# Optimization experiments

Measured on AMD Instinct MI355X. Metric: run time of the kernel, lower is better.

## Reference

```python
import jax, jax.numpy as jnp
import numpy as np

B, N = 32, 512
N_DIM, N_P, N_K = 128, 3, 2
F0_DIM = N_DIM * N_P            # 384
CAT_DIM = N_DIM * (N_K + 1) * N_P  # 1152


def setup_inputs() -> dict:
    key = jax.random.key(0)
    ks = jax.random.split(key, 12)
    s = 0.05
    return {
        "loc": jax.random.uniform(ks[0], (B, N, 2), dtype=jnp.float32),
        "deadline": jax.random.uniform(ks[1], (B, N), dtype=jnp.float32),
        "workload": jax.random.uniform(ks[2], (B, N), dtype=jnp.float32),
        "depot": jax.random.uniform(ks[3], (B, 1, 2), dtype=jnp.float32),
        "W_init": jax.random.normal(ks[4], (3, F0_DIM), dtype=jnp.float32) * s,
        "b_init": jnp.zeros((F0_DIM,), jnp.float32),
        "W_dep": jax.random.normal(ks[5], (2, N_DIM), dtype=jnp.float32) * s,
        "b_dep": jnp.zeros((N_DIM,), jnp.float32),
        "W_g1": jax.random.normal(ks[6], (CAT_DIM, N_DIM), dtype=jnp.float32) * s,
        "b_g1": jnp.zeros((N_DIM,), jnp.float32),
        "W_g2": jax.random.normal(ks[7], (CAT_DIM, N_DIM), dtype=jnp.float32) * s,
        "b_g2": jnp.zeros((N_DIM,), jnp.float32),
        "W_g3": jax.random.normal(ks[8], (CAT_DIM, N_DIM), dtype=jnp.float32) * s,
        "b_g3": jnp.zeros((N_DIM,), jnp.float32),
        "gamma": jnp.ones((F0_DIM,), jnp.float32),
        "beta": jnp.zeros((F0_DIM,), jnp.float32),
        "W_F": jax.random.normal(ks[9], (F0_DIM, N_DIM), dtype=jnp.float32) * s,
        "b_F": jnp.zeros((N_DIM,), jnp.float32),
    }


def _forward(loc, deadline, workload, depot, W_init, b_init, W_dep, b_dep,
             W_g1, b_g1, W_g2, b_g2, W_g3, b_g3, gamma, beta, W_F, b_F):
    # X = [loc, deadline/deadline.max()] -> [B,N,3] (workload is concatenated then dropped in original)
    X = jnp.concatenate([loc, (deadline / deadline.max())[..., None]], axis=-1)
    n = X.shape[1]
    # pairwise squared distances [B,N,N]
    d2 = ((X[:, :, None, :] - X[:, None, :, :]) ** 2).sum(-1)
    off = ~jnp.eye(n, dtype=bool)                      # off-diagonal mask
    d2_safe = jnp.where(off, d2, 1.0)
    A = jnp.where(off, 1.0 / jnp.sqrt(d2_safe), 0.0)   # A = 1/dist off-diag, 0 on diag
    A = jnp.where(jnp.isnan(A), 0.0, A)                # A[A!=A]=0
    A = A / A.max()                                    # global max-normalize
    deg = A.sum(-1) - 1.0                              # (A.sum(-1) - 1)
    L = jnp.eye(n, dtype=A.dtype) * deg[:, None, :] - A  # D - A (diag = deg)
    L2 = L @ L

    F0 = X @ W_init + b_init                           # [B,N,384]
    F0_sq = F0 * F0
    F0_cu = F0 * F0_sq

    def prop(F):
        return jnp.concatenate([F, L @ F, L2 @ F], axis=-1)  # [B,N,1152]

    g1 = prop(F0) @ W_g1 + b_g1
    g2 = prop(F0_sq) @ W_g2 + b_g2
    g3 = prop(F0_cu) @ W_g3 + b_g3
    F1 = jnp.concatenate([g1, g2, g3], axis=-1)        # [B,N,384]
    F1 = jax.nn.leaky_relu(F1) + F0

    # BatchNorm1d (training mode): stats over flattened (B*N) samples, biased var
    flat = F1.reshape(-1, F1.shape[-1])
    mu = flat.mean(0)
    var = ((flat - mu) ** 2).mean(0)
    F1 = (F1 - mu) / jnp.sqrt(var + 1e-5) * gamma + beta

    F_final = jax.nn.leaky_relu(F1 @ W_F + b_F)        # [B,N,128]
    dep = depot @ W_dep + b_dep                        # [B,1,128]
    h = jnp.concatenate([dep, F_final], axis=1)        # [B,N+1,128]
    return h, h.mean(axis=1)


def reference(loc, deadline, workload, depot, W_init, b_init, W_dep, b_dep,
              W_g1, b_g1, W_g2, b_g2, W_g3, b_g3, gamma, beta, W_F, b_F):
    return _forward(loc, deadline, workload, depot, W_init, b_init, W_dep, b_dep,
                    W_g1, b_g1, W_g2, b_g2, W_g3, b_g3, gamma, beta, W_F, b_F)
```

## Files before the change

kernel.cpp:

```cpp
#include <hip/hip_runtime.h>

#define LEAKY(x) ((x) > 0.0f ? (x) : 0.01f * (x))

typedef __attribute__((ext_vector_type(8))) short bf16x8;
typedef __attribute__((ext_vector_type(4))) float f32x4;
typedef __attribute__((ext_vector_type(8))) unsigned short u16x8;
typedef __attribute__((ext_vector_type(4))) unsigned short u16x4;

__device__ __forceinline__ unsigned short f2bf(float f) {
    unsigned int u = __float_as_uint(f);
    unsigned int r = (u + 0x7fffu + ((u >> 16) & 1u)) >> 16;
    return (unsigned short)r;
}
__device__ __forceinline__ float bf2f(unsigned short u) {
    return __uint_as_float(((unsigned int)u) << 16);
}

#define GLD16(gp, lp) __builtin_amdgcn_global_load_lds( \
    (__attribute__((address_space(1))) void*)(gp), \
    (__attribute__((address_space(3))) void*)(lp), 16, 0, 0)


__global__ void k_dmax(const float* __restrict__ deadline, float* __restrict__ dmax) {
    int t = threadIdx.x;
// ... 35 lines not shown
    if (threadIdx.x == 0) {
        float m = fmaxf(fmaxf(smax[0], smax[1]), fmaxf(smax[2], smax[3]));
        atomicMax((unsigned int*)(pmax64 + (blk & 63)), __float_as_uint(m));
    }
}

__global__ __launch_bounds__(256) void k_build(
    const float* __restrict__ loc, const float* __restrict__ deadline,
    const float* __restrict__ dmaxv, const float* __restrict__ rowsum,
    const float* __restrict__ pmax64,
    const float* __restrict__ Wi, const float* __restrict__ bi_,
    const float* __restrict__ Wg1, const float* __restrict__ Wg2, const float* __restrict__ Wg3,
    unsigned short* __restrict__ Lb,
    unsigned short* __restrict__ P1, unsigned short* __restrict__ P2, unsigned short* __restrict__ P3,
    unsigned short* __restrict__ WgT)
{
    __shared__ float amaxS;
    int blk = blockIdx.x;
    int t = threadIdx.x;
    if (blk < 8192) {
        if (t < 64) {
            float m = pmax64[t];
            for (int off = 32; off > 0; off >>= 1) m = fmaxf(m, __shfl_down(m, off));
            if (t == 0) amaxS = m;
        }
        __syncthreads();
        float inv = 1.0f / amaxS;
        float invd = 1.0f / (*dmaxv);
        int id = blk * 256 + t;
        size_t e = (size_t)id * 4;
        size_t bi = e >> 9;
        int b = (int)(bi >> 9);
        int i = (int)(bi & 511);
        int j0 = (int)(e & 511);
        const float* lb = loc + b * 1024;
        const float* db = deadline + b * 512;
        float xi = lb[i * 2], yi = lb[i * 2 + 1], zi = db[i] * invd;
        float4 l01 = *(const float4*)(lb + j0 * 2);
        float4 l23 = *(const float4*)(lb + j0 * 2 + 4);
        float4 dj = *(const float4*)(db + j0);
        float diag = rowsum[bi] * inv - 1.0f;
        float jx[4] = {l01.x, l01.z, l23.x, l23.z};
        float jy[4] = {l01.y, l01.w, l23.y, l23.w};
        float jz[4] = {dj.x * invd, dj.y * invd, dj.z * invd, dj.w * invd};
        u16x4 o;
#pragma unroll
        for (int j = 0; j < 4; j++) {
            float d0 = xi - jx[j], d1 = yi - jy[j], d2 = zi - jz[j];
            float dd = d0 * d0 + d1 * d1 + d2 * d2;
            float v = (i == j0 + j) ? diag : -rsqrtf(dd) * inv;
            o[j] = f2bf(v);
        }
        *(u16x4*)(Lb + e) = o;
    } else if (blk < 14336) {
        int id = (blk - 8192) * 256 + t;
        int row = id / 96, c4 = (id % 96) * 4;
        float x0 = loc[row * 2], x1 = loc[row * 2 + 1], x2 = deadline[row] / (*dmaxv);
        float4 w0 = *(const float4*)(Wi + c4);
        float4 w1 = *(const float4*)(Wi + 384 + c4);
        float4 w2 = *(const float4*)(Wi + 768 + c4);
        float4 bb = *(const float4*)(bi_ + c4);
        float f[4] = {x0 * w0.x + x1 * w1.x + x2 * w2.x + bb.x,
                      x0 * w0.y + x1 * w1.y + x2 * w2.y + bb.y,
                      x0 * w0.z + x1 * w1.z + x2 * w2.z + bb.z,
                      x0 * w0.w + x1 * w1.w + x2 * w2.w + bb.w};
        u16x4 o1, o2, o3;
#pragma unroll
        for (int j = 0; j < 4; j++) {
            o1[j] = f2bf(f[j]); o2[j] = f2bf(f[j] * f[j]); o3[j] = f2bf(f[j] * f[j] * f[j]);
        }
        size_t e = (size_t)row * 384 + c4;
        *(u16x4*)(P1 + e) = o1; *(u16x4*)(P2 + e) = o2; *(u16x4*)(P3 + e) = o3;
    } else {
        int id = (blk - 14336) * 256 + t;
        int part = id / 147456, rem = id % 147456;
        int g = rem / 384, k = rem % 384;
        int kp = g >> 7, n = g & 127;
        const float* W = (kp == 0) ? Wg1 : (kp == 1 ? Wg2 : Wg3);
        WgT[id] = f2bf(W[(part * 384 + k) * 128 + n]);
    }
}


__device__ __forceinline__ void pipe128x128(
    const unsigned short* __restrict__ A0, int As0, const unsigned short* __restrict__ B0, int Bs0, int it0,
    const unsigned short* __restrict__ A1, int As1, const unsigned short* __restrict__ B1, int Bs1, int it1,
    unsigned short* AsL, unsigned short* BsL,
    f32x4 (&acc)[4][4], int t)
{
    const int lane = t & 63, wave = t >> 6;
    const int wm = wave >> 1, wn = wave & 1;
    const int quad = lane >> 4, l16 = lane & 15;
    const int lrow = lane >> 3;
    const int lsw  = ((lane & 7) ^ lrow) * 8;
    const int total = it0 + it1;

    auto stage = [&](int buf, int s) {
        int sg = (s >= it0);
        const unsigned short* A = sg ? A1 : A0;
        const unsigned short* B = sg ? B1 : B0;
        int As = sg ? As1 : As0, Bs = sg ? Bs1 : Bs0;
        int k0 = (sg ? (s - it0) : s) * 64;
#pragma unroll
        for (int j = 0; j < 4; j++) {
            int r0 = wave * 32 + j * 8;
            GLD16(A + (size_t)(r0 + lrow) * As + k0 + lsw, AsL + buf * 8192 + r0 * 64);
            GLD16(B + (size_t)(r0 + lrow) * Bs + k0 + lsw, BsL + buf * 8192 + r0 * 64);
        }
    };

    stage(0, 0);
    if (total > 1) stage(1, 1);
    for (int s = 0; s < total; s++) {
        const int buf = s & 1;
        if (s + 1 < total) asm volatile("s_waitcnt vmcnt(8)" ::: "memory");
        else               asm volatile("s_waitcnt vmcnt(0)" ::: "memory");
        __builtin_amdgcn_s_barrier();
        __builtin_amdgcn_sched_barrier(0);
        bf16x8 af[2][4], bfr[2][4];
#pragma unroll
        for (int h = 0; h < 2; h++) {
            int phys = ((h * 4 + quad) ^ (l16 & 7)) * 8;
#pragma unroll
            for (int i = 0; i < 4; i++)
                af[h][i] = *(const bf16x8*)(AsL + buf * 8192 + (wm * 64 + i * 16 + l16) * 64 + phys);
#pragma unroll
            for (int n = 0; n < 4; n++)
                bfr[h][n] = *(const bf16x8*)(BsL + buf * 8192 + (wn * 64 + n * 16 + l16) * 64 + phys);
        }
        asm volatile("s_waitcnt lgkmcnt(0)" ::: "memory");
        __builtin_amdgcn_sched_barrier(0);
        __builtin_amdgcn_s_barrier();
        __builtin_amdgcn_sched_barrier(0);
        if (s + 2 < total) stage(buf, s + 2);
#pragma unroll
        for (int h = 0; h < 2; h++)
#pragma unroll
            for (int i = 0; i < 4; i++)
#pragma unroll
                for (int n = 0; n < 4; n++)
                    acc[i][n] = __builtin_amdgcn_mfma_f32_16x16x32_bf16(af[h][i], bfr[h][n], acc[i][n], 0, 0, 0);
    }
}

__device__ __forceinline__ void pipe64x64(
    const unsigned short* __restrict__ A0, int As0, const unsigned short* __restrict__ B0, int Bs0, int it0,
    unsigned short* AsL, unsigned short* BsL,
    f32x4 (&acc)[2][2], int t)
{
    const int lane = t & 63, wave = t >> 6;
    const int wm = wave >> 1, wn = wave & 1;
    const int quad = lane >> 4, l16 = lane & 15;
    const int lrow = lane >> 3;
    const int lsw  = ((lane & 7) ^ lrow) * 8;

    auto stage = [&](int buf, int s) {
        int k0 = s * 64;
#pragma unroll
        for (int j = 0; j < 2; j++) {
            int r0 = wave * 16 + j * 8;
            GLD16(A0 + (size_t)(r0 + lrow) * As0 + k0 + lsw, AsL + buf * 4096 + r0 * 64);
            GLD16(B0 + (size_t)(r0 + lrow) * Bs0 + k0 + lsw, BsL + buf * 4096 + r0 * 64);
        }
    };

    stage(0, 0);
    if (it0 > 1) stage(1, 1);
    for (int s = 0; s < it0; s++) {
        const int buf = s & 1;
        if (s + 1 < it0) asm volatile("s_waitcnt vmcnt(4)" ::: "memory");
        else             asm volatile("s_waitcnt vmcnt(0)" ::: "memory");
        __builtin_amdgcn_s_barrier();
        __builtin_amdgcn_sched_barrier(0);
        bf16x8 af[2][2], bfr[2][2];
#pragma unroll
        for (int h = 0; h < 2; h++) {
            int phys = ((h * 4 + quad) ^ (l16 & 7)) * 8;
#pragma unroll
            for (int i = 0; i < 2; i++)
                af[h][i] = *(const bf16x8*)(AsL + buf * 4096 + (wm * 32 + i * 16 + l16) * 64 + phys);
#pragma unroll
            for (int n = 0; n < 2; n++)
                bfr[h][n] = *(const bf16x8*)(BsL + buf * 4096 + (wn * 32 + n * 16 + l16) * 64 + phys);
        }
        asm volatile("s_waitcnt lgkmcnt(0)" ::: "memory");
        __builtin_amdgcn_sched_barrier(0);
        __builtin_amdgcn_s_barrier();
        __builtin_amdgcn_sched_barrier(0);
        if (s + 2 < it0) stage(buf, s + 2);
#pragma unroll
        for (int h = 0; h < 2; h++)
#pragma unroll
            for (int i = 0; i < 2; i++)
#pragma unroll
                for (int n = 0; n < 2; n++)
                    acc[i][n] = __builtin_amdgcn_mfma_f32_16x16x32_bf16(af[h][i], bfr[h][n], acc[i][n], 0, 0, 0);
    }
}

__global__ __launch_bounds__(256) void k_ygemmT(
    const unsigned short* __restrict__ WgT,
    const unsigned short* __restrict__ P1, const unsigned short* __restrict__ P2,
    const unsigned short* __restrict__ P3, unsigned short* __restrict__ Y2T)
{
    __shared__ unsigned short AsL[16384], BsL[16384];
    const int t = threadIdx.x;
    const int id = blockIdx.x;
    const int b = id & 31, tt = id >> 5;
    const int kp = tt >> 2, nb = tt & 3;
    const unsigned short* P = (kp == 0) ? P1 : (kp == 1 ? P2 : P3);
    f32x4 acc[4][4];
#pragma unroll
    for (int i = 0; i < 4; i++)
#pragma unroll
        for (int n = 0; n < 4; n++) acc[i][n] = (f32x4){0.f, 0.f, 0.f, 0.f};
    pipe128x128(WgT + ((size_t)2 * 384 + kp * 128) * 384, 384,
                P + ((size_t)b * 512 + nb * 128) * 384, 384, 6,
                nullptr, 0, nullptr, 0, 0, AsL, BsL, acc, t);

    const int wave = t >> 6, lane = t & 63;
    const int wm = wave >> 1, wn = wave & 1;
    const int quad = lane >> 4, l16 = lane & 15;
#pragma unroll
    for (int i = 0; i < 4; i++)
#pragma unroll
        for (int n = 0; n < 4; n++) {
            int g = kp * 128 + wm * 64 + i * 16 + quad * 4;
            int node = nb * 128 + wn * 64 + n * 16 + l16;
#pragma unroll
            for (int r = 0; r < 4; r++)
                Y2T[((size_t)b * 384 + g + r) * 512 + node] = f2bf(acc[i][n][r]);
        }
}

__global__ __launch_bounds__(256) void k_lg1T(
    const unsigned short* __restrict__ Lb, const unsigned short* __restrict__ Y2T,
    const unsigned short* __restrict__ WgT,
    const unsigned short* __restrict__ P1, const unsigned short* __restrict__ P2,
    const unsigned short* __restrict__ P3, unsigned short* __restrict__ ZT)
{
    __shared__ unsigned short AsL[16384], BsL[16384];
    const int t = threadIdx.x;
    const int id = blockIdx.x;
    const int b = id & 31, tt = id >> 5;
    const int kp = tt >> 2, nb = tt & 3;
    const unsigned short* P = (kp == 0) ? P1 : (kp == 1 ? P2 : P3);
    f32x4 acc[4][4];
#pragma unroll
    for (int i = 0; i < 4; i++)
#pragma unroll
        for (int n = 0; n < 4; n++) acc[i][n] = (f32x4){0.f, 0.f, 0.f, 0.f};
    pipe128x128(Y2T + (size_t)b * 196608 + (size_t)kp * 128 * 512, 512,
                Lb + (size_t)b * 262144 + (size_t)nb * 128 * 512, 512, 8,
                WgT + ((size_t)1 * 384 + kp * 128) * 384, 384,
                P + ((size_t)b * 512 + nb * 128) * 384, 384, 6, AsL, BsL, acc, t);

    const int wave = t >> 6, lane = t & 63;
    const int wm = wave >> 1, wn = wave & 1;
    const int quad = lane >> 4, l16 = lane & 15;
#pragma unroll
    for (int i = 0; i < 4; i++)
#pragma unroll
        for (int n = 0; n < 4; n++) {
            int g = kp * 128 + wm * 64 + i * 16 + quad * 4;
            int node = nb * 128 + wn * 64 + n * 16 + l16;
#pragma unroll
            for (int r = 0; r < 4; r++)
                ZT[((size_t)b * 384 + g + r) * 512 + node] = f2bf(acc[i][n][r]);
        }
}

__global__ __launch_bounds__(256) void k_lg2(
    const unsigned short* __restrict__ Lb, const unsigned short* __restrict__ ZT,
    const unsigned short* __restrict__ WgT,
    const unsigned short* __restrict__ P1, const unsigned short* __restrict__ P2,
    const unsigned short* __restrict__ P3,
    const float* __restrict__ bg1, const float* __restrict__ bg2, const float* __restrict__ bg3,
    unsigned short* __restrict__ F1b, float* __restrict__ bn1, float* __restrict__ bn2)
{
    __shared__ unsigned short AsL[16384], BsL[16384];
    __shared__ float bnS[128], bnQ[128];
    const int t = threadIdx.x;
    const int id = blockIdx.x;
    const int b = id & 31, tt = id >> 5;
    const int mb = tt & 3, gt = tt >> 2;
    if (t < 128) { bnS[t] = 0.f; bnQ[t] = 0.f; }
    const unsigned short* P = (gt == 0) ? P1 : (gt == 1 ? P2 : P3);
    f32x4 acc[4][4];
#pragma unroll
    for (int i = 0; i < 4; i++)
#pragma unroll
        for (int n = 0; n < 4; n++) acc[i][n] = (f32x4){0.f, 0.f, 0.f, 0.f};
    pipe128x128(Lb + (size_t)b * 262144 + (size_t)mb * 128 * 512, 512,
                ZT + (size_t)b * 196608 + (size_t)gt * 128 * 512, 512, 8,
                P + ((size_t)b * 512 + mb * 128) * 384, 384,
                WgT + (size_t)(gt * 128) * 384, 384, 6,
                AsL, BsL, acc, t);

    const int wave = t >> 6, lane = t & 63;
    const int wm = wave >> 1, wn = wave & 1;
    const int quad = lane >> 4, l16 = lane & 15;
    const float* bg = (gt == 0) ? bg1 : (gt == 1 ? bg2 : bg3);
    float ls1[4], ls2[4];
#pragma unroll
    for (int n = 0; n < 4; n++) { ls1[n] = 0.f; ls2[n] = 0.f; }
#pragma unroll
    for (int i = 0; i < 4; i++) {
        int rowl = mb * 128 + wm * 64 + i * 16 + quad * 4;
        size_t rowg = (size_t)b * 512 + rowl;
#pragma unroll
        for (int n = 0; n < 4; n++) {
            int nloc = wn * 64 + n * 16 + l16;
            int g = gt * 128 + nloc;
            float bias = bg[nloc];
#pragma unroll
            for (int r = 0; r < 4; r++) {
                size_t idx = (rowg + r) * 384 + g;
                float c = acc[i][n][r] + bias;
                float v = LEAKY(c) + bf2f(P1[idx]);
                F1b[idx] = f2bf(v);
                ls1[n] += v; ls2[n] += v * v;
            }
        }
    }
#pragma unroll
    for (int n = 0; n < 4; n++) {
        int nloc = wn * 64 + n * 16 + l16;
        atomicAdd(&bnS[nloc], ls1[n]);
        atomicAdd(&bnQ[nloc], ls2[n]);
    }
    __syncthreads();
    if (t < 128) {
        atomicAdd(&bn1[gt * 128 + t], bnS[t]);
        atomicAdd(&bn2[gt * 128 + t], bnQ[t]);
    }
}

__global__ __launch_bounds__(256) void k_bnfold(
    const float* __restrict__ bn1, const float* __restrict__ bn2,
    const float* __restrict__ gamma, const float* __restrict__ beta,
    const float* __restrict__ WF, const float* __restrict__ bF,
    unsigned short* __restrict__ WFsT, float* __restrict__ beffv)
{
    int blk = blockIdx.x;
    if (blk < 192) {
        int id = blk * 256 + threadIdx.x;
        int n = id / 384, k = id % 384;
        float mu = bn1[k] * (1.f / 16384.f);
        float var = bn2[k] * (1.f / 16384.f) - mu * mu;
        float sc = gamma[k] / sqrtf(var + 1e-5f);
        WFsT[id] = f2bf(WF[k * 128 + n] * sc);
    } else {
        __shared__ float ttL[384];
        int c = threadIdx.x;
        for (int k = c; k < 384; k += 256) {
            float mu = bn1[k] * (1.f / 16384.f);
            float var = bn2[k] * (1.f / 16384.f) - mu * mu;
            float sc = gamma[k] / sqrtf(var + 1e-5f);
            ttL[k] = beta[k] - mu * sc;
        }
        __syncthreads();
        if (c < 128) {
            float a = bF[c];
            for (int k = 0; k < 384; k++) a += ttL[k] * WF[k * 128 + c];
            beffv[c] = a;
        }
    }
}

__global__ __launch_bounds__(256) void k_fgemm(
    const unsigned short* __restrict__ F1b, const unsigned short* __restrict__ WFsT,
    const float* __restrict__ beffv, float* __restrict__ out, float* __restrict__ msum)
{
    __shared__ unsigned short AsL[8192], BsL[8192];
    __shared__ float msS[64];
    const int t = threadIdx.x;
    const int id = blockIdx.x;
    const int b = id & 31, tt = id >> 5;
    const int seg = tt >> 1, nt = tt & 1;
    if (t < 64) msS[t] = 0.f;
    f32x4 acc[2][2];
#pragma unroll
    for (int i = 0; i < 2; i++)
#pragma unroll
        for (int n = 0; n < 2; n++) acc[i][n] = (f32x4){0.f, 0.f, 0.f, 0.f};
    pipe64x64(F1b + ((size_t)b * 512 + seg * 64) * 384, 384,
              WFsT + (size_t)nt * 64 * 384, 384, 6, AsL, BsL, acc, t);

    const int wave = t >> 6, lane = t & 63;
    const int wm = wave >> 1, wn = wave & 1;
    const int quad = lane >> 4, l16 = lane & 15;
    float ls[2];
#pragma unroll
    for (int n = 0; n < 2; n++) ls[n] = 0.f;
#pragma unroll
    for (int i = 0; i < 2; i++) {
        int nd = seg * 64 + wm * 32 + i * 16 + quad * 4;
#pragma unroll
        for (int n = 0; n < 2; n++) {
            int col = nt * 64 + wn * 32 + n * 16 + l16;
            float bb = beffv[col];
#pragma unroll
            for (int r = 0; r < 4; r++) {
                float x = acc[i][n][r] + bb;
                float v = LEAKY(x);
                out[(size_t)b * 65664 + (size_t)(nd + r + 1) * 128 + col] = v;
                ls[n] += v;
            }
        }
    }
#pragma unroll
    for (int n = 0; n < 2; n++) atomicAdd(&msS[wn * 32 + n * 16 + l16], ls[n]);
    __syncthreads();
    if (t < 64) atomicAdd(&msum[b * 128 + nt * 64 + t], msS[t]);
}

__global__ void k_meandep(const float* __restrict__ depot, const float* __restrict__ Wd,
                          const float* __restrict__ bd, const float* __restrict__ msum,
                          float* __restrict__ out) {
    int id = blockIdx.x * 256 + threadIdx.x;
    int b = id >> 7, o = id & 127;
    float dep = depot[b * 2] * Wd[o] + depot[b * 2 + 1] * Wd[128 + o] + bd[o];
    out[(size_t)b * 65664 + o] = dep;
    out[2101248 + id] = (msum[id] + dep) * (1.0f / 513.0f);
}


extern "C" void kernel_launch(void* const* d_in, const int* in_sizes, int n_in,
                              void* d_out, int out_size, void* d_ws, size_t ws_size,
                              hipStream_t stream) {
    const float* loc      = (const float*)d_in[0];
    const float* deadline = (const float*)d_in[1];
    const float* depot    = (const float*)d_in[3];
    const float* W_init   = (const float*)d_in[4];
    const float* b_init   = (const float*)d_in[5];
    const float* W_dep    = (const float*)d_in[6];
    const float* b_dep    = (const float*)d_in[7];
    const float* W_g1     = (const float*)d_in[8];
    const float* b_g1     = (const float*)d_in[9];
    const float* W_g2     = (const float*)d_in[10];
    const float* b_g2     = (const float*)d_in[11];
    const float* W_g3     = (const float*)d_in[12];
    const float* b_g3     = (const float*)d_in[13];
    const float* gamma    = (const float*)d_in[14];
    const float* beta     = (const float*)d_in[15];
    const float* W_F      = (const float*)d_in[16];
    const float* b_F      = (const float*)d_in[17];
    float* out = (float*)d_out;
    float* ws  = (float*)d_ws;

    float* dmaxv  = ws + 0;
    float* pmax64 = ws + 4;
    float* bn1    = ws + 68;
    float* bn2    = ws + 452;
    float* msum   = ws + 836;
    float* rowsum = ws + 4932;
    float* beffv  = ws + 21316;
    unsigned short* Lb   = (unsigned short*)(ws + 21448);
    unsigned short* P1   = (unsigned short*)(ws + 4215752);
    unsigned short* P2   = (unsigned short*)(ws + 7361480);
    unsigned short* P3   = (unsigned short*)(ws + 10507208);
    unsigned short* WgT  = (unsigned short*)(ws + 13652936);
    unsigned short* WFsT = (unsigned short*)(ws + 13874120);
    unsigned short* Y2T  = (unsigned short*)(ws + 13898696);
    unsigned short* ZT   = (unsigned short*)(ws + 17044424);
    unsigned short* F1b  = (unsigned short*)(ws + 20190152);

    hipMemsetAsync(ws, 0, 4932 * sizeof(float), stream);

    k_dmax<<<64, 256, 0, stream>>>(deadline, dmaxv);
    k_rowstats<<<4096, 256, 0, stream>>>(loc, deadline, dmaxv, rowsum, pmax64);
    k_build<<<16064, 256, 0, stream>>>(loc, deadline, dmaxv, rowsum, pmax64,
                                       W_init, b_init, W_g1, W_g2, W_g3,
                                       Lb, P1, P2, P3, WgT);

    k_ygemmT<<<384, 256, 0, stream>>>(WgT, P1, P2, P3, Y2T);
    k_lg1T<<<384, 256, 0, stream>>>(Lb, Y2T, WgT, P1, P2, P3, ZT);
    k_lg2<<<384, 256, 0, stream>>>(Lb, ZT, WgT, P1, P2, P3,
                                   b_g1, b_g2, b_g3, F1b, bn1, bn2);

    k_bnfold<<<193, 256, 0, stream>>>(bn1, bn2, gamma, beta, W_F, b_F, WFsT, beffv);
    k_fgemm<<<512, 256, 0, stream>>>(F1b, WFsT, beffv, out, msum);
    k_meandep<<<16, 256, 0, stream>>>(depot, W_dep, b_dep, msum, out);
}
```

Measured before the change: 222.6 us.

## Split 128x128 GEMM tiles across 8 waves with MFMA operand swap and setprio

The three graph-propagation GEMM kernels now launch 512 threads (8 waves) per 128x128 tile instead of 256. Each wave computes a 32x64 sub-tile and issues half as many global-to-LDS loads per stage, with the vmcnt waits adjusted to match. For the transposed-output kernels, the MFMA operands are swapped so each lane holds four consecutive nodes, which allows a single vectorized 4-element bf16 store in place of four strided scalar stores. s_setprio is raised around the MFMA bursts to favour the math waves over the load-issuing ones. The aim is better latency hiding with only 384 blocks on the device, at the cost of lower per-wave register reuse and more barrier participants.

```diff
diff --git a/kernel.cpp b/kernel.cpp
--- a/kernel.cpp
+++ b/kernel.cpp
@@ -141,11 +141,12 @@
 }
 
 
+template <bool SWAP>
 __device__ __forceinline__ void pipe128x128(
     const unsigned short* __restrict__ A0, int As0, const unsigned short* __restrict__ B0, int Bs0, int it0,
     const unsigned short* __restrict__ A1, int As1, const unsigned short* __restrict__ B1, int Bs1, int it1,
     unsigned short* AsL, unsigned short* BsL,
-    f32x4 (&acc)[4][4], int t)
+    f32x4 (&acc)[2][4], int t)
 {
     const int lane = t & 63, wave = t >> 6;
     const int wm = wave >> 1, wn = wave & 1;
@@ -161,8 +162,8 @@
         int As = sg ? As1 : As0, Bs = sg ? Bs1 : Bs0;
         int k0 = (sg ? (s - it0) : s) * 64;
 #pragma unroll
-        for (int j = 0; j < 4; j++) {
-            int r0 = wave * 32 + j * 8;
+        for (int j = 0; j < 2; j++) {
+            int r0 = wave * 16 + j * 8;
             GLD16(A + (size_t)(r0 + lrow) * As + k0 + lsw, AsL + buf * 8192 + r0 * 64);
             GLD16(B + (size_t)(r0 + lrow) * Bs + k0 + lsw, BsL + buf * 8192 + r0 * 64);
         }
@@ -172,17 +173,17 @@
     if (total > 1) stage(1, 1);
     for (int s = 0; s < total; s++) {
         const int buf = s & 1;
-        if (s + 1 < total) asm volatile("s_waitcnt vmcnt(8)" ::: "memory");
+        if (s + 1 < total) asm volatile("s_waitcnt vmcnt(4)" ::: "memory");
         else               asm volatile("s_waitcnt vmcnt(0)" ::: "memory");
         __builtin_amdgcn_s_barrier();
         __builtin_amdgcn_sched_barrier(0);
-        bf16x8 af[2][4], bfr[2][4];
+        bf16x8 af[2][2], bfr[2][4];
 #pragma unroll
         for (int h = 0; h < 2; h++) {
             int phys = ((h * 4 + quad) ^ (l16 & 7)) * 8;
 #pragma unroll
-            for (int i = 0; i < 4; i++)
-                af[h][i] = *(const bf16x8*)(AsL + buf * 8192 + (wm * 64 + i * 16 + l16) * 64 + phys);
+            for (int i = 0; i < 2; i++)
+                af[h][i] = *(const bf16x8*)(AsL + buf * 8192 + (wm * 32 + i * 16 + l16) * 64 + phys);
 #pragma unroll
             for (int n = 0; n < 4; n++)
                 bfr[h][n] = *(const bf16x8*)(BsL + buf * 8192 + (wn * 64 + n * 16 + l16) * 64 + phys);
@@ -192,13 +193,17 @@
         __builtin_amdgcn_s_barrier();
         __builtin_amdgcn_sched_barrier(0);
         if (s + 2 < total) stage(buf, s + 2);
+        __builtin_amdgcn_s_setprio(1);
 #pragma unroll
         for (int h = 0; h < 2; h++)
 #pragma unroll
-            for (int i = 0; i < 4; i++)
+            for (int i = 0; i < 2; i++)
 #pragma unroll
                 for (int n = 0; n < 4; n++)
-                    acc[i][n] = __builtin_amdgcn_mfma_f32_16x16x32_bf16(af[h][i], bfr[h][n], acc[i][n], 0, 0, 0);
+                    acc[i][n] = SWAP
+                        ? __builtin_amdgcn_mfma_f32_16x16x32_bf16(bfr[h][n], af[h][i], acc[i][n], 0, 0, 0)
+                        : __builtin_amdgcn_mfma_f32_16x16x32_bf16(af[h][i], bfr[h][n], acc[i][n], 0, 0, 0);
+        __builtin_amdgcn_s_setprio(0);
     }
 }
 
@@ -247,6 +252,7 @@
         __builtin_amdgcn_s_barrier();
         __builtin_amdgcn_sched_barrier(0);
         if (s + 2 < it0) stage(buf, s + 2);
+        __builtin_amdgcn_s_setprio(1);
 #pragma unroll
         for (int h = 0; h < 2; h++)
 #pragma unroll
@@ -254,10 +260,11 @@
 #pragma unroll
                 for (int n = 0; n < 2; n++)
                     acc[i][n] = __builtin_amdgcn_mfma_f32_16x16x32_bf16(af[h][i], bfr[h][n], acc[i][n], 0, 0, 0);
-    }
-}
-
-__global__ __launch_bounds__(256) void k_ygemmT(
+        __builtin_amdgcn_s_setprio(0);
+    }
+}
+
+__global__ __launch_bounds__(512, 4) void k_ygemmT(
     const unsigned short* __restrict__ WgT,
     const unsigned short* __restrict__ P1, const unsigned short* __restrict__ P2,
     const unsigned short* __restrict__ P3, unsigned short* __restrict__ Y2T)
@@ -268,31 +275,33 @@
     const int b = id & 31, tt = id >> 5;
     const int kp = tt >> 2, nb = tt & 3;
     const unsigned short* P = (kp == 0) ? P1 : (kp == 1 ? P2 : P3);
-    f32x4 acc[4][4];
-#pragma unroll
-    for (int i = 0; i < 4; i++)
+    f32x4 acc[2][4];
+#pragma unroll
+    for (int i = 0; i < 2; i++)
 #pragma unroll
         for (int n = 0; n < 4; n++) acc[i][n] = (f32x4){0.f, 0.f, 0.f, 0.f};
-    pipe128x128(WgT + ((size_t)2 * 384 + kp * 128) * 384, 384,
-                P + ((size_t)b * 512 + nb * 128) * 384, 384, 6,
-                nullptr, 0, nullptr, 0, 0, AsL, BsL, acc, t);
+    pipe128x128<true>(WgT + ((size_t)2 * 384 + kp * 128) * 384, 384,
+                      P + ((size_t)b * 512 + nb * 128) * 384, 384, 6,
+                      nullptr, 0, nullptr, 0, 0, AsL, BsL, acc, t);
 
     const int wave = t >> 6, lane = t & 63;
     const int wm = wave >> 1, wn = wave & 1;
     const int quad = lane >> 4, l16 = lane & 15;
 #pragma unroll
-    for (int i = 0; i < 4; i++)
+    for (int i = 0; i < 2; i++) {
+        int g = kp * 128 + wm * 32 + i * 16 + l16;
 #pragma unroll
         for (int n = 0; n < 4; n++) {
-            int g = kp * 128 + wm * 64 + i * 16 + quad * 4;
-            int node = nb * 128 + wn * 64 + n * 16 + l16;
-#pragma unroll
-            for (int r = 0; r < 4; r++)
-                Y2T[((size_t)b * 384 + g + r) * 512 + node] = f2bf(acc[i][n][r]);
-        }
-}
-
-__global__ __launch_bounds__(256) void k_lg1T(
+            int node = nb * 128 + wn * 64 + n * 16 + quad * 4;
+            u16x4 o;
+#pragma unroll
+            for (int r = 0; r < 4; r++) o[r] = f2bf(acc[i][n][r]);
+            *(u16x4*)(Y2T + ((size_t)b * 384 + g) * 512 + node) = o;
+        }
+    }
+}
+
+__global__ __launch_bounds__(512, 4) void k_lg1T(
     const unsigned short* __restrict__ Lb, const unsigned short* __restrict__ Y2T,
     const unsigned short* __restrict__ WgT,
     const unsigned short* __restrict__ P1, const unsigned short* __restrict__ P2,
@@ -304,32 +313,34 @@
     const int b = id & 31, tt = id >> 5;
     const int kp = tt >> 2, nb = tt & 3;
     const unsigned short* P = (kp == 0) ? P1 : (kp == 1 ? P2 : P3);
-    f32x4 acc[4][4];
-#pragma unroll
-    for (int i = 0; i < 4; i++)
+    f32x4 acc[2][4];
+#pragma unroll
+    for (int i = 0; i < 2; i++)
 #pragma unroll
         for (int n = 0; n < 4; n++) acc[i][n] = (f32x4){0.f, 0.f, 0.f, 0.f};
-    pipe128x128(Y2T + (size_t)b * 196608 + (size_t)kp * 128 * 512, 512,
-                Lb + (size_t)b * 262144 + (size_t)nb * 128 * 512, 512, 8,
-                WgT + ((size_t)1 * 384 + kp * 128) * 384, 384,
-                P + ((size_t)b * 512 + nb * 128) * 384, 384, 6, AsL, BsL, acc, t);
+    pipe128x128<true>(Y2T + (size_t)b * 196608 + (size_t)kp * 128 * 512, 512,
+                      Lb + (size_t)b * 262144 + (size_t)nb * 128 * 512, 512, 8,
+                      WgT + ((size_t)1 * 384 + kp * 128) * 384, 384,
+                      P + ((size_t)b * 512 + nb * 128) * 384, 384, 6, AsL, BsL, acc, t);
 
     const int wave = t >> 6, lane = t & 63;
     const int wm = wave >> 1, wn = wave & 1;
     const int quad = lane >> 4, l16 = lane & 15;
 #pragma unroll
-    for (int i = 0; i < 4; i++)
+    for (int i = 0; i < 2; i++) {
+        int g = kp * 128 + wm * 32 + i * 16 + l16;
 #pragma unroll
         for (int n = 0; n < 4; n++) {
-            int g = kp * 128 + wm * 64 + i * 16 + quad * 4;
-            int node = nb * 128 + wn * 64 + n * 16 + l16;
-#pragma unroll
-            for (int r = 0; r < 4; r++)
-                ZT[((size_t)b * 384 + g + r) * 512 + node] = f2bf(acc[i][n][r]);
-        }
-}
-
-__global__ __launch_bounds__(256) void k_lg2(
+            int node = nb * 128 + wn * 64 + n * 16 + quad * 4;
+            u16x4 o;
+#pragma unroll
+            for (int r = 0; r < 4; r++) o[r] = f2bf(acc[i][n][r]);
+            *(u16x4*)(ZT + ((size_t)b * 384 + g) * 512 + node) = o;
+        }
+    }
+}
+
+__global__ __launch_bounds__(512, 4) void k_lg2(
     const unsigned short* __restrict__ Lb, const unsigned short* __restrict__ ZT,
     const unsigned short* __restrict__ WgT,
     const unsigned short* __restrict__ P1, const unsigned short* __restrict__ P2,
@@ -345,16 +356,16 @@
     const int mb = tt & 3, gt = tt >> 2;
     if (t < 128) { bnS[t] = 0.f; bnQ[t] = 0.f; }
     const unsigned short* P = (gt == 0) ? P1 : (gt == 1 ? P2 : P3);
-    f32x4 acc[4][4];
-#pragma unroll
-    for (int i = 0; i < 4; i++)
+    f32x4 acc[2][4];
+#pragma unroll
+    for (int i = 0; i < 2; i++)
 #pragma unroll
         for (int n = 0; n < 4; n++) acc[i][n] = (f32x4){0.f, 0.f, 0.f, 0.f};
-    pipe128x128(Lb + (size_t)b * 262144 + (size_t)mb * 128 * 512, 512,
-                ZT + (size_t)b * 196608 + (size_t)gt * 128 * 512, 512, 8,
-                P + ((size_t)b * 512 + mb * 128) * 384, 384,
-                WgT + (size_t)(gt * 128) * 384, 384, 6,
-                AsL, BsL, acc, t);
+    pipe128x128<false>(Lb + (size_t)b * 262144 + (size_t)mb * 128 * 512, 512,
+                       ZT + (size_t)b * 196608 + (size_t)gt * 128 * 512, 512, 8,
+                       P + ((size_t)b * 512 + mb * 128) * 384, 384,
+                       WgT + (size_t)(gt * 128) * 384, 384, 6,
+                       AsL, BsL, acc, t);
 
     const int wave = t >> 6, lane = t & 63;
     const int wm = wave >> 1, wn = wave & 1;
@@ -364,8 +375,8 @@
 #pragma unroll
     for (int n = 0; n < 4; n++) { ls1[n] = 0.f; ls2[n] = 0.f; }
 #pragma unroll
-    for (int i = 0; i < 4; i++) {
-        int rowl = mb * 128 + wm * 64 + i * 16 + quad * 4;
+    for (int i = 0; i < 2; i++) {
+        int rowl = mb * 128 + wm * 32 + i * 16 + quad * 4;
         size_t rowg = (size_t)b * 512 + rowl;
 #pragma unroll
         for (int n = 0; n < 4; n++) {
@@ -533,9 +544,9 @@
                                        W_init, b_init, W_g1, W_g2, W_g3,
                                        Lb, P1, P2, P3, WgT);
 
-    k_ygemmT<<<384, 256, 0, stream>>>(WgT, P1, P2, P3, Y2T);
-    k_lg1T<<<384, 256, 0, stream>>>(Lb, Y2T, WgT, P1, P2, P3, ZT);
-    k_lg2<<<384, 256, 0, stream>>>(Lb, ZT, WgT, P1, P2, P3,
+    k_ygemmT<<<384, 512, 0, stream>>>(WgT, P1, P2, P3, Y2T);
+    k_lg1T<<<384, 512, 0, stream>>>(Lb, Y2T, WgT, P1, P2, P3, ZT);
+    k_lg2<<<384, 512, 0, stream>>>(Lb, ZT, WgT, P1, P2, P3,
                                    b_g1, b_g2, b_g3, F1b, bn1, bn2);
 
     k_bnfold<<<193, 256, 0, stream>>>(bn1, bn2, gamma, beta, W_F, b_F, WFsT, beffv);
```

Measured after the change: 230.5 us. +3.5%, slower.

## Precompute all three weight-projection products in one launch and add them in epilogues

Applied to the files above, without the earlier changes.

All three W·P projections (parts 0, 1 and 2) now come from a single wider kernel, k_wp, with 1152 blocks. The Laplacian GEMMs therefore no longer chain a second K-segment through the pipeline. They add the precomputed Y1/Y0 terms in their epilogues, and swapped MFMA operand order gives vectorized u16x4 stores. This removes the dual-segment pipeline logic and lets the weight GEMMs run with more parallelism. In exchange it adds extra global writes and reads of two bf16 intermediates (Y1T aliases F1b, Y0T is a new buffer) and an additional bf16 rounding before the sum.

```diff
diff --git a/kernel.cpp b/kernel.cpp
--- a/kernel.cpp
+++ b/kernel.cpp
@@ -141,9 +141,9 @@
 }
 
 
+template <bool SWAP>
 __device__ __forceinline__ void pipe128x128(
     const unsigned short* __restrict__ A0, int As0, const unsigned short* __restrict__ B0, int Bs0, int it0,
-    const unsigned short* __restrict__ A1, int As1, const unsigned short* __restrict__ B1, int Bs1, int it1,
     unsigned short* AsL, unsigned short* BsL,
     f32x4 (&acc)[4][4], int t)
 {
@@ -152,28 +152,23 @@
     const int quad = lane >> 4, l16 = lane & 15;
     const int lrow = lane >> 3;
     const int lsw  = ((lane & 7) ^ lrow) * 8;
-    const int total = it0 + it1;
 
     auto stage = [&](int buf, int s) {
-        int sg = (s >= it0);
-        const unsigned short* A = sg ? A1 : A0;
-        const unsigned short* B = sg ? B1 : B0;
-        int As = sg ? As1 : As0, Bs = sg ? Bs1 : Bs0;
-        int k0 = (sg ? (s - it0) : s) * 64;
+        int k0 = s * 64;
 #pragma unroll
         for (int j = 0; j < 4; j++) {
             int r0 = wave * 32 + j * 8;
-            GLD16(A + (size_t)(r0 + lrow) * As + k0 + lsw, AsL + buf * 8192 + r0 * 64);
-            GLD16(B + (size_t)(r0 + lrow) * Bs + k0 + lsw, BsL + buf * 8192 + r0 * 64);
+            GLD16(A0 + (size_t)(r0 + lrow) * As0 + k0 + lsw, AsL + buf * 8192 + r0 * 64);
+            GLD16(B0 + (size_t)(r0 + lrow) * Bs0 + k0 + lsw, BsL + buf * 8192 + r0 * 64);
         }
     };
 
     stage(0, 0);
-    if (total > 1) stage(1, 1);
-    for (int s = 0; s < total; s++) {
+    if (it0 > 1) stage(1, 1);
+    for (int s = 0; s < it0; s++) {
         const int buf = s & 1;
-        if (s + 1 < total) asm volatile("s_waitcnt vmcnt(8)" ::: "memory");
-        else               asm volatile("s_waitcnt vmcnt(0)" ::: "memory");
+        if (s + 1 < it0) asm volatile("s_waitcnt vmcnt(8)" ::: "memory");
+        else             asm volatile("s_waitcnt vmcnt(0)" ::: "memory");
         __builtin_amdgcn_s_barrier();
         __builtin_amdgcn_sched_barrier(0);
         bf16x8 af[2][4], bfr[2][4];
@@ -191,14 +186,16 @@
         __builtin_amdgcn_sched_barrier(0);
         __builtin_amdgcn_s_barrier();
         __builtin_amdgcn_sched_barrier(0);
-        if (s + 2 < total) stage(buf, s + 2);
+        if (s + 2 < it0) stage(buf, s + 2);
 #pragma unroll
         for (int h = 0; h < 2; h++)
 #pragma unroll
             for (int i = 0; i < 4; i++)
 #pragma unroll
                 for (int n = 0; n < 4; n++)
-                    acc[i][n] = __builtin_amdgcn_mfma_f32_16x16x32_bf16(af[h][i], bfr[h][n], acc[i][n], 0, 0, 0);
+                    acc[i][n] = SWAP
+                        ? __builtin_amdgcn_mfma_f32_16x16x32_bf16(bfr[h][n], af[h][i], acc[i][n], 0, 0, 0)
+                        : __builtin_amdgcn_mfma_f32_16x16x32_bf16(af[h][i], bfr[h][n], acc[i][n], 0, 0, 0);
     }
 }
 
@@ -257,83 +254,88 @@
     }
 }
 
-__global__ __launch_bounds__(256) void k_ygemmT(
+__global__ __launch_bounds__(256) void k_wp(
     const unsigned short* __restrict__ WgT,
     const unsigned short* __restrict__ P1, const unsigned short* __restrict__ P2,
-    const unsigned short* __restrict__ P3, unsigned short* __restrict__ Y2T)
+    const unsigned short* __restrict__ P3,
+    unsigned short* __restrict__ Y0T, unsigned short* __restrict__ Y1T,
+    unsigned short* __restrict__ Y2T)
+{
+    __shared__ unsigned short AsL[16384], BsL[16384];
+    const int t = threadIdx.x;
+    const int id = blockIdx.x;
+    const int b = id & 31, tt = id >> 5;
+    const int kp = tt / 12, rem = tt % 12;
+    const int part = rem >> 2, nb = rem & 3;
+    const unsigned short* P = (kp == 0) ? P1 : (kp == 1 ? P2 : P3);
+    unsigned short* Y = (part == 2) ? Y2T : (part == 1 ? Y1T : Y0T);
+    f32x4 acc[4][4];
+#pragma unroll
+    for (int i = 0; i < 4; i++)
+#pragma unroll
+        for (int n = 0; n < 4; n++) acc[i][n] = (f32x4){0.f, 0.f, 0.f, 0.f};
+    pipe128x128<true>(WgT + ((size_t)part * 384 + kp * 128) * 384, 384,
+                      P + ((size_t)b * 512 + nb * 128) * 384, 384, 6,
+                      AsL, BsL, acc, t);
+
+    const int wave = t >> 6, lane = t & 63;
+    const int wm = wave >> 1, wn = wave & 1;
+    const int quad = lane >> 4, l16 = lane & 15;
+#pragma unroll
+    for (int i = 0; i < 4; i++) {
+        int g = kp * 128 + wm * 64 + i * 16 + l16;
+#pragma unroll
+        for (int n = 0; n < 4; n++) {
+            int node = nb * 128 + wn * 64 + n * 16 + quad * 4;
+            u16x4 o;
+#pragma unroll
+            for (int r = 0; r < 4; r++) o[r] = f2bf(acc[i][n][r]);
+            *(u16x4*)(Y + ((size_t)b * 384 + g) * 512 + node) = o;
+        }
+    }
+}
+
+__global__ __launch_bounds__(256) void k_lg1T(
+    const unsigned short* __restrict__ Lb, const unsigned short* __restrict__ Y2T,
+    const unsigned short* __restrict__ Y1T, unsigned short* __restrict__ ZT)
 {
     __shared__ unsigned short AsL[16384], BsL[16384];
     const int t = threadIdx.x;
     const int id = blockIdx.x;
     const int b = id & 31, tt = id >> 5;
     const int kp = tt >> 2, nb = tt & 3;
-    const unsigned short* P = (kp == 0) ? P1 : (kp == 1 ? P2 : P3);
     f32x4 acc[4][4];
 #pragma unroll
     for (int i = 0; i < 4; i++)
 #pragma unroll
         for (int n = 0; n < 4; n++) acc[i][n] = (f32x4){0.f, 0.f, 0.f, 0.f};
-    pipe128x128(WgT + ((size_t)2 * 384 + kp * 128) * 384, 384,
-                P + ((size_t)b * 512 + nb * 128) * 384, 384, 6,
-                nullptr, 0, nullptr, 0, 0, AsL, BsL, acc, t);
+    pipe128x128<true>(Y2T + (size_t)b * 196608 + (size_t)kp * 128 * 512, 512,
+                      Lb + (size_t)b * 262144 + (size_t)nb * 128 * 512, 512, 8,
+                      AsL, BsL, acc, t);
 
     const int wave = t >> 6, lane = t & 63;
     const int wm = wave >> 1, wn = wave & 1;
     const int quad = lane >> 4, l16 = lane & 15;
 #pragma unroll
-    for (int i = 0; i < 4; i++)
+    for (int i = 0; i < 4; i++) {
+        int g = kp * 128 + wm * 64 + i * 16 + l16;
 #pragma unroll
         for (int n = 0; n < 4; n++) {
-            int g = kp * 128 + wm * 64 + i * 16 + quad * 4;
-            int node = nb * 128 + wn * 64 + n * 16 + l16;
-#pragma unroll
-            for (int r = 0; r < 4; r++)
-                Y2T[((size_t)b * 384 + g + r) * 512 + node] = f2bf(acc[i][n][r]);
-        }
-}
-
-__global__ __launch_bounds__(256) void k_lg1T(
-    const unsigned short* __restrict__ Lb, const unsigned short* __restrict__ Y2T,
-    const unsigned short* __restrict__ WgT,
-    const unsigned short* __restrict__ P1, const unsigned short* __restrict__ P2,
-    const unsigned short* __restrict__ P3, unsigned short* __restrict__ ZT)
-{
-    __shared__ unsigned short AsL[16384], BsL[16384];
-    const int t = threadIdx.x;
-    const int id = blockIdx.x;
-    const int b = id & 31, tt = id >> 5;
-    const int kp = tt >> 2, nb = tt & 3;
-    const unsigned short* P = (kp == 0) ? P1 : (kp == 1 ? P2 : P3);
-    f32x4 acc[4][4];
-#pragma unroll
-    for (int i = 0; i < 4; i++)
-#pragma unroll
-        for (int n = 0; n < 4; n++) acc[i][n] = (f32x4){0.f, 0.f, 0.f, 0.f};
-    pipe128x128(Y2T + (size_t)b * 196608 + (size_t)kp * 128 * 512, 512,
-                Lb + (size_t)b * 262144 + (size_t)nb * 128 * 512, 512, 8,
-                WgT + ((size_t)1 * 384 + kp * 128) * 384, 384,
-                P + ((size_t)b * 512 + nb * 128) * 384, 384, 6, AsL, BsL, acc, t);
-
-    const int wave = t >> 6, lane = t & 63;
-    const int wm = wave >> 1, wn = wave & 1;
-    const int quad = lane >> 4, l16 = lane & 15;
-#pragma unroll
-    for (int i = 0; i < 4; i++)
-#pragma unroll
-        for (int n = 0; n < 4; n++) {
-            int g = kp * 128 + wm * 64 + i * 16 + quad * 4;
-            int node = nb * 128 + wn * 64 + n * 16 + l16;
-#pragma unroll
-            for (int r = 0; r < 4; r++)
-                ZT[((size_t)b * 384 + g + r) * 512 + node] = f2bf(acc[i][n][r]);
-        }
+            int node = nb * 128 + wn * 64 + n * 16 + quad * 4;
+            size_t addr = ((size_t)b * 384 + g) * 512 + node;
+            u16x4 y1 = *(const u16x4*)(Y1T + addr);
+            u16x4 o;
+#pragma unroll
+            for (int r = 0; r < 4; r++) o[r] = f2bf(acc[i][n][r] + bf2f(y1[r]));
+            *(u16x4*)(ZT + addr) = o;
+        }
+    }
 }
 
 __global__ __launch_bounds__(256) void k_lg2(
     const unsigned short* __restrict__ Lb, const unsigned short* __restrict__ ZT,
-    const unsigned short* __restrict__ WgT,
-    const unsigned short* __restrict__ P1, const unsigned short* __restrict__ P2,
-    const unsigned short* __restrict__ P3,
+    const unsigned short* __restrict__ Y0T,
+    const unsigned short* __restrict__ P1,
     const float* __restrict__ bg1, const float* __restrict__ bg2, const float* __restrict__ bg3,
     unsigned short* __restrict__ F1b, float* __restrict__ bn1, float* __restrict__ bn2)
 {
@@ -344,17 +346,14 @@
     const int b = id & 31, tt = id >> 5;
     const int mb = tt & 3, gt = tt >> 2;
     if (t < 128) { bnS[t] = 0.f; bnQ[t] = 0.f; }
-    const unsigned short* P = (gt == 0) ? P1 : (gt == 1 ? P2 : P3);
     f32x4 acc[4][4];
 #pragma unroll
     for (int i = 0; i < 4; i++)
 #pragma unroll
         for (int n = 0; n < 4; n++) acc[i][n] = (f32x4){0.f, 0.f, 0.f, 0.f};
-    pipe128x128(Lb + (size_t)b * 262144 + (size_t)mb * 128 * 512, 512,
-                ZT + (size_t)b * 196608 + (size_t)gt * 128 * 512, 512, 8,
-                P + ((size_t)b * 512 + mb * 128) * 384, 384,
-                WgT + (size_t)(gt * 128) * 384, 384, 6,
-                AsL, BsL, acc, t);
+    pipe128x128<false>(Lb + (size_t)b * 262144 + (size_t)mb * 128 * 512, 512,
+                       ZT + (size_t)b * 196608 + (size_t)gt * 128 * 512, 512, 8,
+                       AsL, BsL, acc, t);
 
     const int wave = t >> 6, lane = t & 63;
     const int wm = wave >> 1, wn = wave & 1;
@@ -372,10 +371,11 @@
             int nloc = wn * 64 + n * 16 + l16;
             int g = gt * 128 + nloc;
             float bias = bg[nloc];
+            u16x4 y0 = *(const u16x4*)(Y0T + ((size_t)b * 384 + g) * 512 + rowl);
 #pragma unroll
             for (int r = 0; r < 4; r++) {
                 size_t idx = (rowg + r) * 384 + g;
-                float c = acc[i][n][r] + bias;
+                float c = acc[i][n][r] + bf2f(y0[r]) + bias;
                 float v = LEAKY(c) + bf2f(P1[idx]);
                 F1b[idx] = f2bf(v);
                 ls1[n] += v; ls2[n] += v * v;
@@ -524,6 +524,8 @@
     unsigned short* Y2T  = (unsigned short*)(ws + 13898696);
     unsigned short* ZT   = (unsigned short*)(ws + 17044424);
     unsigned short* F1b  = (unsigned short*)(ws + 20190152);
+    unsigned short* Y1T  = F1b;
+    unsigned short* Y0T  = (unsigned short*)(ws + 23335880);
 
     hipMemsetAsync(ws, 0, 4932 * sizeof(float), stream);
 
@@ -533,9 +535,9 @@
                                        W_init, b_init, W_g1, W_g2, W_g3,
                                        Lb, P1, P2, P3, WgT);
 
-    k_ygemmT<<<384, 256, 0, stream>>>(WgT, P1, P2, P3, Y2T);
-    k_lg1T<<<384, 256, 0, stream>>>(Lb, Y2T, WgT, P1, P2, P3, ZT);
-    k_lg2<<<384, 256, 0, stream>>>(Lb, ZT, WgT, P1, P2, P3,
+    k_wp<<<1152, 256, 0, stream>>>(WgT, P1, P2, P3, Y0T, Y1T, Y2T);
+    k_lg1T<<<384, 256, 0, stream>>>(Lb, Y2T, Y1T, ZT);
+    k_lg2<<<384, 256, 0, stream>>>(Lb, ZT, Y0T, P1,
                                    b_g1, b_g2, b_g3, F1b, bn1, bn2);
 
     k_bnfold<<<193, 256, 0, stream>>>(bn1, bn2, gamma, beta, W_F, b_F, WFsT, beffv);
```

New measurement: 231.8 us. +4.1%, slower.

## Shrink GEMM tiles to 128x64 to double grid size; vectorize transposed stores

Applied to the files above, without the earlier changes.

The three chained Laplacian GEMM kernels now use 128x64 output tiles instead of 128x128, which doubles each launch from 384 to 768 blocks so the 256 CUs on MI355X are better filled. The shared-memory B buffer is halved to match, and the vmcnt wait count is adjusted for the smaller loads. For the two transposed-output kernels, the MFMA operands are swapped so each lane holds four consecutive nodes, letting the stores be 8-byte vector writes instead of scattered 2-byte writes. The cost is lower arithmetic intensity per block, so more A-tile traffic is reloaded from memory or cache.

```diff
diff --git a/kernel.cpp b/kernel.cpp
--- a/kernel.cpp
+++ b/kernel.cpp
@@ -141,11 +141,12 @@
 }
 
 
-__device__ __forceinline__ void pipe128x128(
+template <bool SWAP>
+__device__ __forceinline__ void pipe128x64(
     const unsigned short* __restrict__ A0, int As0, const unsigned short* __restrict__ B0, int Bs0, int it0,
     const unsigned short* __restrict__ A1, int As1, const unsigned short* __restrict__ B1, int Bs1, int it1,
     unsigned short* AsL, unsigned short* BsL,
-    f32x4 (&acc)[4][4], int t)
+    f32x4 (&acc)[4][2], int t)
 {
     const int lane = t & 63, wave = t >> 6;
     const int wm = wave >> 1, wn = wave & 1;
@@ -164,7 +165,11 @@
         for (int j = 0; j < 4; j++) {
             int r0 = wave * 32 + j * 8;
             GLD16(A + (size_t)(r0 + lrow) * As + k0 + lsw, AsL + buf * 8192 + r0 * 64);
-            GLD16(B + (size_t)(r0 + lrow) * Bs + k0 + lsw, BsL + buf * 8192 + r0 * 64);
+        }
+#pragma unroll
+        for (int j = 0; j < 2; j++) {
+            int r0 = wave * 16 + j * 8;
+            GLD16(B + (size_t)(r0 + lrow) * Bs + k0 + lsw, BsL + buf * 4096 + r0 * 64);
         }
     };
 
@@ -172,11 +177,11 @@
     if (total > 1) stage(1, 1);
     for (int s = 0; s < total; s++) {
         const int buf = s & 1;
-        if (s + 1 < total) asm volatile("s_waitcnt vmcnt(8)" ::: "memory");
+        if (s + 1 < total) asm volatile("s_waitcnt vmcnt(6)" ::: "memory");
         else               asm volatile("s_waitcnt vmcnt(0)" ::: "memory");
         __builtin_amdgcn_s_barrier();
         __builtin_amdgcn_sched_barrier(0);
-        bf16x8 af[2][4], bfr[2][4];
+        bf16x8 af[2][4], bfr[2][2];
 #pragma unroll
         for (int h = 0; h < 2; h++) {
             int phys = ((h * 4 + quad) ^ (l16 & 7)) * 8;
@@ -184,8 +189,8 @@
             for (int i = 0; i < 4; i++)
                 af[h][i] = *(const bf16x8*)(AsL + buf * 8192 + (wm * 64 + i * 16 + l16) * 64 + phys);
 #pragma unroll
-            for (int n = 0; n < 4; n++)
-                bfr[h][n] = *(const bf16x8*)(BsL + buf * 8192 + (wn * 64 + n * 16 + l16) * 64 + phys);
+            for (int n = 0; n < 2; n++)
+                bfr[h][n] = *(const bf16x8*)(BsL + buf * 4096 + (wn * 32 + n * 16 + l16) * 64 + phys);
         }
         asm volatile("s_waitcnt lgkmcnt(0)" ::: "memory");
         __builtin_amdgcn_sched_barrier(0);
@@ -197,8 +202,10 @@
 #pragma unroll
             for (int i = 0; i < 4; i++)
 #pragma unroll
-                for (int n = 0; n < 4; n++)
-                    acc[i][n] = __builtin_amdgcn_mfma_f32_16x16x32_bf16(af[h][i], bfr[h][n], acc[i][n], 0, 0, 0);
+                for (int n = 0; n < 2; n++)
+                    acc[i][n] = SWAP
+                        ? __builtin_amdgcn_mfma_f32_16x16x32_bf16(bfr[h][n], af[h][i], acc[i][n], 0, 0, 0)
+                        : __builtin_amdgcn_mfma_f32_16x16x32_bf16(af[h][i], bfr[h][n], acc[i][n], 0, 0, 0);
     }
 }
 
@@ -262,34 +269,36 @@
     const unsigned short* __restrict__ P1, const unsigned short* __restrict__ P2,
     const unsigned short* __restrict__ P3, unsigned short* __restrict__ Y2T)
 {
-    __shared__ unsigned short AsL[16384], BsL[16384];
+    __shared__ unsigned short AsL[16384], BsL[8192];
     const int t = threadIdx.x;
     const int id = blockIdx.x;
     const int b = id & 31, tt = id >> 5;
-    const int kp = tt >> 2, nb = tt & 3;
+    const int kp = tt >> 3, nb = tt & 7;
     const unsigned short* P = (kp == 0) ? P1 : (kp == 1 ? P2 : P3);
-    f32x4 acc[4][4];
+    f32x4 acc[4][2];
 #pragma unroll
     for (int i = 0; i < 4; i++)
 #pragma unroll
-        for (int n = 0; n < 4; n++) acc[i][n] = (f32x4){0.f, 0.f, 0.f, 0.f};
-    pipe128x128(WgT + ((size_t)2 * 384 + kp * 128) * 384, 384,
-                P + ((size_t)b * 512 + nb * 128) * 384, 384, 6,
-                nullptr, 0, nullptr, 0, 0, AsL, BsL, acc, t);
+        for (int n = 0; n < 2; n++) acc[i][n] = (f32x4){0.f, 0.f, 0.f, 0.f};
+    pipe128x64<true>(WgT + ((size_t)2 * 384 + kp * 128) * 384, 384,
+                     P + ((size_t)b * 512 + nb * 64) * 384, 384, 6,
+                     nullptr, 0, nullptr, 0, 0, AsL, BsL, acc, t);
 
     const int wave = t >> 6, lane = t & 63;
     const int wm = wave >> 1, wn = wave & 1;
     const int quad = lane >> 4, l16 = lane & 15;
 #pragma unroll
-    for (int i = 0; i < 4; i++)
-#pragma unroll
-        for (int n = 0; n < 4; n++) {
-            int g = kp * 128 + wm * 64 + i * 16 + quad * 4;
-            int node = nb * 128 + wn * 64 + n * 16 + l16;
-#pragma unroll
-            for (int r = 0; r < 4; r++)
-                Y2T[((size_t)b * 384 + g + r) * 512 + node] = f2bf(acc[i][n][r]);
-        }
+    for (int i = 0; i < 4; i++) {
+        int g = kp * 128 + wm * 64 + i * 16 + l16;
+#pragma unroll
+        for (int n = 0; n < 2; n++) {
+            int node = nb * 64 + wn * 32 + n * 16 + quad * 4;
+            u16x4 o;
+#pragma unroll
+            for (int r = 0; r < 4; r++) o[r] = f2bf(acc[i][n][r]);
+            *(u16x4*)(Y2T + ((size_t)b * 384 + g) * 512 + node) = o;
+        }
+    }
 }
 
 __global__ __launch_bounds__(256) void k_lg1T(
@@ -298,35 +307,37 @@
     const unsigned short* __restrict__ P1, const unsigned short* __restrict__ P2,
     const unsigned short* __restrict__ P3, unsigned short* __restrict__ ZT)
 {
-    __shared__ unsigned short AsL[16384], BsL[16384];
+    __shared__ unsigned short AsL[16384], BsL[8192];
     const int t = threadIdx.x;
     const int id = blockIdx.x;
     const int b = id & 31, tt = id >> 5;
-    const int kp = tt >> 2, nb = tt & 3;
+    const int kp = tt >> 3, nb = tt & 7;
     const unsigned short* P = (kp == 0) ? P1 : (kp == 1 ? P2 : P3);
-    f32x4 acc[4][4];
+    f32x4 acc[4][2];
 #pragma unroll
     for (int i = 0; i < 4; i++)
 #pragma unroll
-        for (int n = 0; n < 4; n++) acc[i][n] = (f32x4){0.f, 0.f, 0.f, 0.f};
-    pipe128x128(Y2T + (size_t)b * 196608 + (size_t)kp * 128 * 512, 512,
-                Lb + (size_t)b * 262144 + (size_t)nb * 128 * 512, 512, 8,
-                WgT + ((size_t)1 * 384 + kp * 128) * 384, 384,
-                P + ((size_t)b * 512 + nb * 128) * 384, 384, 6, AsL, BsL, acc, t);
+        for (int n = 0; n < 2; n++) acc[i][n] = (f32x4){0.f, 0.f, 0.f, 0.f};
+    pipe128x64<true>(Y2T + (size_t)b * 196608 + (size_t)kp * 128 * 512, 512,
+                     Lb + (size_t)b * 262144 + (size_t)nb * 64 * 512, 512, 8,
+                     WgT + ((size_t)1 * 384 + kp * 128) * 384, 384,
+                     P + ((size_t)b * 512 + nb * 64) * 384, 384, 6, AsL, BsL, acc, t);
 
     const int wave = t >> 6, lane = t & 63;
     const int wm = wave >> 1, wn = wave & 1;
     const int quad = lane >> 4, l16 = lane & 15;
 #pragma unroll
-    for (int i = 0; i < 4; i++)
-#pragma unroll
-        for (int n = 0; n < 4; n++) {
-            int g = kp * 128 + wm * 64 + i * 16 + quad * 4;
-            int node = nb * 128 + wn * 64 + n * 16 + l16;
-#pragma unroll
-            for (int r = 0; r < 4; r++)
-                ZT[((size_t)b * 384 + g + r) * 512 + node] = f2bf(acc[i][n][r]);
-        }
+    for (int i = 0; i < 4; i++) {
+        int g = kp * 128 + wm * 64 + i * 16 + l16;
+#pragma unroll
+        for (int n = 0; n < 2; n++) {
+            int node = nb * 64 + wn * 32 + n * 16 + quad * 4;
+            u16x4 o;
+#pragma unroll
+            for (int r = 0; r < 4; r++) o[r] = f2bf(acc[i][n][r]);
+            *(u16x4*)(ZT + ((size_t)b * 384 + g) * 512 + node) = o;
+        }
+    }
 }
 
 __global__ __launch_bounds__(256) void k_lg2(
@@ -337,41 +348,42 @@
     const float* __restrict__ bg1, const float* __restrict__ bg2, const float* __restrict__ bg3,
     unsigned short* __restrict__ F1b, float* __restrict__ bn1, float* __restrict__ bn2)
 {
-    __shared__ unsigned short AsL[16384], BsL[16384];
-    __shared__ float bnS[128], bnQ[128];
+    __shared__ unsigned short AsL[16384], BsL[8192];
+    __shared__ float bnS[64], bnQ[64];
     const int t = threadIdx.x;
     const int id = blockIdx.x;
     const int b = id & 31, tt = id >> 5;
     const int mb = tt & 3, gt = tt >> 2;
-    if (t < 128) { bnS[t] = 0.f; bnQ[t] = 0.f; }
-    const unsigned short* P = (gt == 0) ? P1 : (gt == 1 ? P2 : P3);
-    f32x4 acc[4][4];
+    const int kp = gt >> 1;
+    if (t < 64) { bnS[t] = 0.f; bnQ[t] = 0.f; }
+    const unsigned short* P = (kp == 0) ? P1 : (kp == 1 ? P2 : P3);
+    f32x4 acc[4][2];
 #pragma unroll
     for (int i = 0; i < 4; i++)
 #pragma unroll
-        for (int n = 0; n < 4; n++) acc[i][n] = (f32x4){0.f, 0.f, 0.f, 0.f};
-    pipe128x128(Lb + (size_t)b * 262144 + (size_t)mb * 128 * 512, 512,
-                ZT + (size_t)b * 196608 + (size_t)gt * 128 * 512, 512, 8,
-                P + ((size_t)b * 512 + mb * 128) * 384, 384,
-                WgT + (size_t)(gt * 128) * 384, 384, 6,
-                AsL, BsL, acc, t);
+        for (int n = 0; n < 2; n++) acc[i][n] = (f32x4){0.f, 0.f, 0.f, 0.f};
+    pipe128x64<false>(Lb + (size_t)b * 262144 + (size_t)mb * 128 * 512, 512,
+                      ZT + (size_t)b * 196608 + (size_t)gt * 64 * 512, 512, 8,
+                      P + ((size_t)b * 512 + mb * 128) * 384, 384,
+                      WgT + (size_t)(gt * 64) * 384, 384, 6,
+                      AsL, BsL, acc, t);
 
     const int wave = t >> 6, lane = t & 63;
     const int wm = wave >> 1, wn = wave & 1;
     const int quad = lane >> 4, l16 = lane & 15;
-    const float* bg = (gt == 0) ? bg1 : (gt == 1 ? bg2 : bg3);
-    float ls1[4], ls2[4];
-#pragma unroll
-    for (int n = 0; n < 4; n++) { ls1[n] = 0.f; ls2[n] = 0.f; }
+    const float* bg = (kp == 0) ? bg1 : (kp == 1 ? bg2 : bg3);
+    float ls1[2], ls2[2];
+#pragma unroll
+    for (int n = 0; n < 2; n++) { ls1[n] = 0.f; ls2[n] = 0.f; }
 #pragma unroll
     for (int i = 0; i < 4; i++) {
         int rowl = mb * 128 + wm * 64 + i * 16 + quad * 4;
         size_t rowg = (size_t)b * 512 + rowl;
 #pragma unroll
-        for (int n = 0; n < 4; n++) {
-            int nloc = wn * 64 + n * 16 + l16;
-            int g = gt * 128 + nloc;
-            float bias = bg[nloc];
+        for (int n = 0; n < 2; n++) {
+            int nloc = wn * 32 + n * 16 + l16;
+            int g = gt * 64 + nloc;
+            float bias = bg[(gt & 1) * 64 + nloc];
 #pragma unroll
             for (int r = 0; r < 4; r++) {
                 size_t idx = (rowg + r) * 384 + g;
@@ -383,15 +395,15 @@
         }
     }
 #pragma unroll
-    for (int n = 0; n < 4; n++) {
-        int nloc = wn * 64 + n * 16 + l16;
+    for (int n = 0; n < 2; n++) {
+        int nloc = wn * 32 + n * 16 + l16;
         atomicAdd(&bnS[nloc], ls1[n]);
         atomicAdd(&bnQ[nloc], ls2[n]);
     }
     __syncthreads();
-    if (t < 128) {
-        atomicAdd(&bn1[gt * 128 + t], bnS[t]);
-        atomicAdd(&bn2[gt * 128 + t], bnQ[t]);
+    if (t < 64) {
+        atomicAdd(&bn1[gt * 64 + t], bnS[t]);
+        atomicAdd(&bn2[gt * 64 + t], bnQ[t]);
     }
 }
 
@@ -533,9 +545,9 @@
                                        W_init, b_init, W_g1, W_g2, W_g3,
                                        Lb, P1, P2, P3, WgT);
 
-    k_ygemmT<<<384, 256, 0, stream>>>(WgT, P1, P2, P3, Y2T);
-    k_lg1T<<<384, 256, 0, stream>>>(Lb, Y2T, WgT, P1, P2, P3, ZT);
-    k_lg2<<<384, 256, 0, stream>>>(Lb, ZT, WgT, P1, P2, P3,
+    k_ygemmT<<<768, 256, 0, stream>>>(WgT, P1, P2, P3, Y2T);
+    k_lg1T<<<768, 256, 0, stream>>>(Lb, Y2T, WgT, P1, P2, P3, ZT);
+    k_lg2<<<768, 256, 0, stream>>>(Lb, ZT, WgT, P1, P2, P3,
                                    b_g1, b_g2, b_g3, F1b, bn1, bn2);
 
     k_bnfold<<<193, 256, 0, stream>>>(bn1, bn2, gamma, beta, W_F, b_F, WFsT, beffv);
```

Result: slower. 229.8 us (+3.2%).
